# Performance work log

Measured on AMD Instinct MI355X. Metric: run time of the kernel, lower is better.

Reference implementation:

```python
import jax, jax.numpy as jnp
import numpy as np

STRIDE = (1, 1)
PADDING = ((1, 1), (1, 1))


def setup_inputs() -> dict:
    key = jax.random.key(0)
    kx, kw, kb = jax.random.split(key, 3)
    x = jax.random.normal(kx, (32, 128, 56, 56), dtype=jnp.float32)
    weight = jax.random.normal(kw, (256, 128, 3, 3), dtype=jnp.float32)  # (O, I, kh, kw)
    bias = jax.random.normal(kb, (256,), dtype=jnp.float32)
    return {"x": x, "weight": weight, "bias": bias}


def reference(x, weight, bias):
    # Faithful dense 2D convolution (cross-correlation, as in the torch module),
    # NCHW input, OIHW weight, stride 1, padding 1.
    out = jax.lax.conv_general_dilated(
        x, weight,
        window_strides=STRIDE,
        padding=PADDING,
        dimension_numbers=("NCHW", "OIHW", "NCHW"),
    )
    return out + bias[None, :, None, None]
```

## Files before the change

### kernel.cpp

```cpp
#include <hip/hip_runtime.h>

#define C_IN   128
#define H_IN   56
#define W_IN   56
#define HW     3136
#define CHW    401408
#define O_OUT  256
#define OHW    802816

#define BM 256
#define BN 128
#define BK 64
#define LDK 72

typedef __bf16 bf16x8 __attribute__((ext_vector_type(8)));
typedef float  f32x4  __attribute__((ext_vector_type(4)));
typedef unsigned short ushort_t;
typedef ushort_t ushort8 __attribute__((ext_vector_type(8)));

__device__ __forceinline__ ushort_t f2bf(float f) {
    union { float f; unsigned u; } v; v.f = f;
    unsigned r = (v.u + 0x7fffu + ((v.u >> 16) & 1u)) >> 16;
    return (ushort_t)r;
}

__global__ void wt_kernel(const float* __restrict__ w, ushort_t* __restrict__ wbf) {
    int idx = blockIdx.x * 256 + threadIdx.x;
    if (idx >= 9 * 256 * 128) return;
    int pos = idx >> 15;
    int rem = idx & 32767;
    int o   = rem >> 7;
    int c   = rem & 127;
    wbf[idx] = f2bf(w[o * 1152 + c * 9 + pos]);
}

__global__ __launch_bounds__(512, 4)
void conv_kernel(const float* __restrict__ x, const ushort_t* __restrict__ wbf,
                 const float* __restrict__ bias, float* __restrict__ out) {
    __shared__ ushort_t As[BM * LDK];
    __shared__ ushort_t Bs[BN * LDK];

    const int tid  = threadIdx.x;
    const int lane = tid & 63;
    const int wave = tid >> 6;
    const int wm   = wave >> 1;
    const int wn   = wave & 1;
    const int l15  = lane & 15;
    const int quad = lane >> 4;

    const int pix_base = blockIdx.x * BN;

    const int px  = tid & 127;
    const int cg0 = tid >> 7;
    const int p   = pix_base + px;
    const int n_img = p / HW;
    const int hw    = p - n_img * HW;
    const int h     = hw / W_IN;
    const int w_    = hw - h * W_IN;
    const float* ximg = x + (long)n_img * CHW;

    f32x4 acc[4][4];
    #pragma unroll
    for (int t = 0; t < 4; ++t)
        #pragma unroll
        for (int u = 0; u < 4; ++u)
            acc[t][u] = f32x4{0.f, 0.f, 0.f, 0.f};

    for (int pos = 0; pos < 9; ++pos) {
        const int dh = pos / 3 - 1;
        const int dw = pos - (pos / 3) * 3 - 1;
        const int ih = h + dh;
        const int iw = w_ + dw;
        const bool valid = ((unsigned)ih < (unsigned)H_IN) && ((unsigned)iw < (unsigned)W_IN);
        const float* xsrc = ximg + ih * W_IN + iw;

        for (int half = 0; half < 2; ++half) {
            const int c0 = half * 64;

            {
                const ushort_t* wsrc = wbf + ((pos * 256) << 7) + c0;
                #pragma unroll
                for (int s = 0; s < 4; ++s) {
                    const int o  = (tid >> 3) + s * 64;
                    const int cg = tid & 7;
                    ushort8 v = *(const ushort8*)(wsrc + (o << 7) + cg * 8);
                    *(ushort8*)(&As[o * LDK + cg * 8]) = v;
                }
            }
            {
                #pragma unroll
                for (int s = 0; s < 2; ++s) {
                    const int cg = cg0 + s * 4;
                    const float* src = xsrc + (long)(c0 + cg * 8) * HW;
                    ushort8 v;
                    #pragma unroll
                    for (int j = 0; j < 8; ++j) {
                        float f = valid ? src[j * HW] : 0.0f;
                        v[j] = f2bf(f);
                    }
                    *(ushort8*)(&Bs[px * LDK + cg * 8]) = v;
                }
            }
            __syncthreads();

            #pragma unroll
            for (int ks = 0; ks < 2; ++ks) {
                bf16x8 af[4], bfv[4];
                #pragma unroll
                for (int t = 0; t < 4; ++t) {
                    const int row = wm * 64 + t * 16 + l15;
                    af[t] = *(const bf16x8*)(&As[row * LDK + ks * 32 + quad * 8]);
                }
                #pragma unroll
                for (int u = 0; u < 4; ++u) {
                    const int col = wn * 64 + u * 16 + l15;
                    bfv[u] = *(const bf16x8*)(&Bs[col * LDK + ks * 32 + quad * 8]);
                }
                #pragma unroll
                for (int t = 0; t < 4; ++t)
                    #pragma unroll
                    for (int u = 0; u < 4; ++u)
                        acc[t][u] = __builtin_amdgcn_mfma_f32_16x16x32_bf16(af[t], bfv[u], acc[t][u], 0, 0, 0);
            }
            __syncthreads();
        }
    }

    #pragma unroll
    for (int u = 0; u < 4; ++u) {
        const int col = wn * 64 + u * 16 + l15;
        const int pp  = pix_base + col;
        const int nn  = pp / HW;
        const int hw2 = pp - nn * HW;
        const long obase = (long)nn * OHW + hw2;
        #pragma unroll
        for (int t = 0; t < 4; ++t) {
            const int o_base = wm * 64 + t * 16 + quad * 4;
            #pragma unroll
            for (int r = 0; r < 4; ++r) {
                const int o = o_base + r;
                out[obase + (long)o * HW] = acc[t][u][r] + bias[o];
            }
        }
    }
}

extern "C" void kernel_launch(void* const* d_in, const int* in_sizes, int n_in,
                              void* d_out, int out_size, void* d_ws, size_t ws_size,
                              hipStream_t stream) {
    const float* x    = (const float*)d_in[0];
    const float* w    = (const float*)d_in[1];
    const float* bias = (const float*)d_in[2];
    float* out        = (float*)d_out;
    ushort_t* wbf     = (ushort_t*)d_ws;

    hipLaunchKernelGGL(wt_kernel, dim3(1152), dim3(256), 0, stream, w, wbf);
    hipLaunchKernelGGL(conv_kernel, dim3(100352 / BN), dim3(512), 0, stream, x, wbf, bias, out);
}
```

Baseline: 237.8 us.

## Pre-convert input to NHWC bf16 and load swizzled LDS tiles in conv

After: 779.6 us. 3.28x slower.

```diff
diff --git a/kernel.cpp b/kernel.cpp
--- a/kernel.cpp
+++ b/kernel.cpp
@@ -10,7 +10,7 @@
 
 #define BM 256
 #define BN 128
-#define BK 64
+#define LDSW 64
 #define LDK 72
 
 typedef __bf16 bf16x8 __attribute__((ext_vector_type(8)));
@@ -34,11 +34,24 @@
     wbf[idx] = f2bf(w[o * 1152 + c * 9 + pos]);
 }
 
-__global__ __launch_bounds__(512, 4)
-void conv_kernel(const float* __restrict__ x, const ushort_t* __restrict__ wbf,
-                 const float* __restrict__ bias, float* __restrict__ out) {
-    __shared__ ushort_t As[BM * LDK];
-    __shared__ ushort_t Bs[BN * LDK];
+__global__ void xt_kernel(const float* __restrict__ x, ushort_t* __restrict__ xb) {
+    int idx = blockIdx.x * 256 + threadIdx.x;
+    int p  = idx >> 4;
+    int cg = idx & 15;
+    int n  = p / HW;
+    int hw = p - n * HW;
+    const float* src = x + (long)n * CHW + (long)(cg * 8) * HW + hw;
+    ushort8 v;
+    #pragma unroll
+    for (int j = 0; j < 8; ++j) v[j] = f2bf(src[j * HW]);
+    *(ushort8*)(xb + (long)p * 128 + cg * 8) = v;
+}
+
+__global__ __launch_bounds__(512, 6)
+void conv2_kernel(const ushort_t* __restrict__ xb, const ushort_t* __restrict__ wbf,
+                  const float* __restrict__ bias, float* __restrict__ out) {
+    __shared__ ushort_t As[BM * LDSW];
+    __shared__ ushort_t Bs[BN * LDSW];
 
     const int tid  = threadIdx.x;
     const int lane = tid & 63;
@@ -50,6 +63,115 @@
 
     const int pix_base = blockIdx.x * BN;
 
+    const int bpx = tid >> 2;
+    const int bg0 = (tid & 3) * 2;
+    const int p   = pix_base + bpx;
+    const int n_img = p / HW;
+    const int hw    = p - n_img * HW;
+    const int h     = hw / W_IN;
+    const int w_    = hw - h * W_IN;
+
+    const int ao = tid >> 3;
+    const int ag = tid & 7;
+
+    f32x4 acc[4][4];
+    #pragma unroll
+    for (int t = 0; t < 4; ++t)
+        #pragma unroll
+        for (int u = 0; u < 4; ++u)
+            acc[t][u] = f32x4{0.f, 0.f, 0.f, 0.f};
+
+    for (int pos = 0; pos < 9; ++pos) {
+        const int dh = pos / 3 - 1;
+        const int dw = pos - (pos / 3) * 3 - 1;
+        const int ih = h + dh;
+        const int iw = w_ + dw;
+        const bool valid = ((unsigned)ih < (unsigned)H_IN) && ((unsigned)iw < (unsigned)W_IN);
+        const ushort_t* bsrc = xb + (long)(p + dh * W_IN + dw) * 128;
+
+        #pragma unroll
+        for (int half = 0; half < 2; ++half) {
+            const int c0 = half * 64;
+
+            {
+                const ushort_t* wsrc = wbf + pos * 32768 + c0;
+                #pragma unroll
+                for (int s = 0; s < 4; ++s) {
+                    const int o = ao + s * 64;
+                    ushort8 v = *(const ushort8*)(wsrc + (o << 7) + ag * 8);
+                    *(ushort8*)(&As[o * LDSW + ((ag ^ (o & 7)) * 8)]) = v;
+                }
+            }
+            {
+                #pragma unroll
+                for (int q = 0; q < 2; ++q) {
+                    const int g = bg0 + q;
+                    ushort8 v;
+                    if (valid) v = *(const ushort8*)(bsrc + c0 + g * 8);
+                    else       v = ushort8{0,0,0,0,0,0,0,0};
+                    *(ushort8*)(&Bs[bpx * LDSW + ((g ^ (bpx & 7)) * 8)]) = v;
+                }
+            }
+            __syncthreads();
+
+            #pragma unroll
+            for (int ks = 0; ks < 2; ++ks) {
+                bf16x8 af[4], bfv[4];
+                const int k16 = ks * 4 + quad;
+                #pragma unroll
+                for (int t = 0; t < 4; ++t) {
+                    const int row = wm * 64 + t * 16 + l15;
+                    af[t] = *(const bf16x8*)(&As[row * LDSW + ((k16 ^ (row & 7)) * 8)]);
+                }
+                #pragma unroll
+                for (int u = 0; u < 4; ++u) {
+                    const int col = wn * 64 + u * 16 + l15;
+                    bfv[u] = *(const bf16x8*)(&Bs[col * LDSW + ((k16 ^ (col & 7)) * 8)]);
+                }
+                #pragma unroll
+                for (int t = 0; t < 4; ++t)
+                    #pragma unroll
+                    for (int u = 0; u < 4; ++u)
+                        acc[t][u] = __builtin_amdgcn_mfma_f32_16x16x32_bf16(af[t], bfv[u], acc[t][u], 0, 0, 0);
+            }
+            __syncthreads();
+        }
+    }
+
+    #pragma unroll
+    for (int u = 0; u < 4; ++u) {
+        const int col = wn * 64 + u * 16 + l15;
+        const int pp  = pix_base + col;
+        const int nn  = pp / HW;
+        const int hw2 = pp - nn * HW;
+        const long obase = (long)nn * OHW + hw2;
+        #pragma unroll
+        for (int t = 0; t < 4; ++t) {
+            const int o_base = wm * 64 + t * 16 + quad * 4;
+            #pragma unroll
+            for (int r = 0; r < 4; ++r) {
+                const int o = o_base + r;
+                out[obase + (long)o * HW] = acc[t][u][r] + bias[o];
+            }
+        }
+    }
+}
+
+__global__ __launch_bounds__(512, 4)
+void conv_kernel(const float* __restrict__ x, const ushort_t* __restrict__ wbf,
+                 const float* __restrict__ bias, float* __restrict__ out) {
+    __shared__ ushort_t As[BM * LDK];
+    __shared__ ushort_t Bs[BN * LDK];
+
+    const int tid  = threadIdx.x;
+    const int lane = tid & 63;
+    const int wave = tid >> 6;
+    const int wm   = wave >> 1;
+    const int wn   = wave & 1;
+    const int l15  = lane & 15;
+    const int quad = lane >> 4;
+
+    const int pix_base = blockIdx.x * BN;
     const int px  = tid & 127;
     const int cg0 = tid >> 7;
     const int p   = pix_base + px;
@@ -76,7 +198,6 @@
 
         for (int half = 0; half < 2; ++half) {
             const int c0 = half * 64;
-
             {
                 const ushort_t* wsrc = wbf + ((pos * 256) << 7) + c0;
                 #pragma unroll
@@ -152,8 +273,19 @@
     const float* w    = (const float*)d_in[1];
     const float* bias = (const float*)d_in[2];
     float* out        = (float*)d_out;
-    ushort_t* wbf     = (ushort_t*)d_ws;
+
+    ushort_t* wbf = (ushort_t*)d_ws;
+    ushort_t* xb  = (ushort_t*)((char*)d_ws + 589824);
+
+    const size_t need = 589824u + 25690112u;
 
     hipLaunchKernelGGL(wt_kernel, dim3(1152), dim3(256), 0, stream, w, wbf);
-    hipLaunchKernelGGL(conv_kernel, dim3(100352 / BN), dim3(512), 0, stream, x, wbf, bias, out);
-}
+    if (ws_size >= need) {
+        hipLaunchKernelGGL(xt_kernel, dim3(6272), dim3(256), 0, stream, x, xb);
+        hipLaunchKernelGGL(conv2_kernel, dim3(100352 / BN), dim3(512), 0, stream,
+                           xb, wbf, bias, out);
+    } else {
+        hipLaunchKernelGGL(conv_kernel, dim3(100352 / BN), dim3(512), 0, stream,
+                           x, wbf, bias, out);
+    }
+}
```
